# Optimization experiments

Hardware: AMD Instinct MI355X
Metric: run time of the kernel (lower is better)

The kernel has to match this reference:

```python
import jax, jax.numpy as jnp
import numpy as np

B, C, P, NP = 16, 768, 2048, 64
FFE = 4


def _ln(x, g, b, eps=1e-5):
    m = jnp.mean(x, axis=-1, keepdims=True)
    v = jnp.mean(jnp.square(x - m), axis=-1, keepdims=True)
    return (x - m) * jax.lax.rsqrt(v + eps) * g + b


def _gelu(x):
    return jax.nn.gelu(x, approximate=False)  # torch nn.GELU default (erf)


def _any_attn(q, k, v, nqg, nqb, nkg, nkb, nvg, nvb, wq, wk, wv, wp, bq, bk, bv, bp):
    # AnyAttention: LN each stream, project, ReLU-gated logits scaled by d^-0.5, softmax, proj
    scale = q.shape[-1] ** -0.5
    qn = _ln(q, nqg, nqb) @ wq + bq
    kn = _ln(k, nkg, nkb) @ wk + bk
    vn = _ln(v, nvg, nvb) @ wv + bv
    attn = jnp.einsum('bqc,bkc->bqk', qn, kn)
    attn = jax.nn.relu(attn) * scale  # returned attn is relu*scale (pre-softmax)
    out = jnp.einsum('bqk,bkc->bqc', jax.nn.softmax(attn, axis=-1), vn)
    return attn, out @ wp + bp


def _forward(x, parts,
             enc_nq_g, enc_nq_b, enc_nk_g, enc_nk_b, enc_nv_g, enc_nv_b,
             enc_wq, enc_wk, enc_wv, enc_wp, enc_bq, enc_bk, enc_bv, enc_bp,
             dec_nq_g, dec_nq_b, dec_nk_g, dec_nk_b, dec_nv_g, dec_nv_b,
             dec_wq, dec_wk, dec_wv, dec_wp, dec_bq, dec_bk, dec_bv, dec_bp,
             ffn_ng, ffn_nb, ffn_w1, ffn_b1, ffn_w2, ffn_b2,
             sr_w1, sr_b1, sr_w2, sr_b2):
    x = jnp.swapaxes(x, 1, 2)  # b c p -> b p c
    # SimpleReasoning: SE-style gate over part tokens (AdaptiveMaxPool1d(1) = max over channel dim)
    g = jnp.max(parts, axis=-1)                                  # [b, np]
    g = _gelu(g @ sr_w1 + sr_b1)
    gate = jax.nn.sigmoid(g @ sr_w2 + sr_b2)[..., None]          # [b, np, 1]
    parts = gate * parts + parts                                 # parts1 + parts (residual)
    # enc_attn: parts attend over image tokens
    attn0, attn_out = _any_attn(parts, x, x,
                                enc_nq_g, enc_nq_b, enc_nk_g, enc_nk_b, enc_nv_g, enc_nv_b,
                                enc_wq, enc_wk, enc_wv, enc_wp, enc_bq, enc_bk, enc_bv, enc_bp)
    attn_0 = jnp.max(attn0, axis=-1)                             # maxpool over k -> [b, np]
    parts_in = parts + attn_out
    # FFN on image tokens with residual
    h = _ln(x, ffn_ng, ffn_nb)
    feats1 = x + (_gelu(h @ ffn_w1 + ffn_b1) @ ffn_w2 + ffn_b2)
    # dec_attn: image tokens attend over part tokens
    _, feats = _any_attn(feats1, parts_in, parts_in,
                         dec_nq_g, dec_nq_b, dec_nk_g, dec_nk_b, dec_nv_g, dec_nv_b,
                         dec_wq, dec_wk, dec_wv, dec_wp, dec_bq, dec_bk, dec_bv, dec_bp)
    feats = x + feats
    return jnp.swapaxes(feats, 1, 2), attn_0                     # [b, c, p], [b, np]


def setup_inputs() -> dict:
    key = jax.random.key(0)
    ki = iter(jax.random.split(key, 48))
    def rn(shape, s=1.0):
        return jax.random.normal(next(ki), shape, jnp.float32) * s
    d = {}
    d['x'] = rn((B, C, P))
    d['parts'] = rn((B, NP, C))
    for pre in ('enc', 'dec'):
        for nm in ('nq', 'nk', 'nv'):
            d[f'{pre}_{nm}_g'] = jnp.ones((C,), jnp.float32)
            d[f'{pre}_{nm}_b'] = jnp.zeros((C,), jnp.float32)
        for nm in ('wq', 'wk', 'wv', 'wp'):
            d[f'{pre}_{nm}'] = rn((C, C), 0.02)
        for nm in ('bq', 'bk', 'bv', 'bp'):
            d[f'{pre}_{nm}'] = jnp.zeros((C,), jnp.float32)
    d['ffn_ng'] = jnp.ones((C,), jnp.float32)
    d['ffn_nb'] = jnp.zeros((C,), jnp.float32)
    d['ffn_w1'] = rn((C, FFE * C), 0.02)
    d['ffn_b1'] = jnp.zeros((FFE * C,), jnp.float32)
    d['ffn_w2'] = rn((FFE * C, C), 0.02)
    d['ffn_b2'] = jnp.zeros((C,), jnp.float32)
    d['sr_w1'] = rn((NP, NP), 0.1)
    d['sr_b1'] = jnp.zeros((NP,), jnp.float32)
    d['sr_w2'] = rn((NP, NP), 0.1)
    d['sr_b2'] = jnp.zeros((NP,), jnp.float32)
    return d


def reference(x, parts,
              enc_nq_g, enc_nq_b, enc_nk_g, enc_nk_b, enc_nv_g, enc_nv_b,
              enc_wq, enc_wk, enc_wv, enc_wp, enc_bq, enc_bk, enc_bv, enc_bp,
              dec_nq_g, dec_nq_b, dec_nk_g, dec_nk_b, dec_nv_g, dec_nv_b,
              dec_wq, dec_wk, dec_wv, dec_wp, dec_bq, dec_bk, dec_bv, dec_bp,
              ffn_ng, ffn_nb, ffn_w1, ffn_b1, ffn_w2, ffn_b2,
              sr_w1, sr_b1, sr_w2, sr_b2):
    return _forward(x, parts,
                    enc_nq_g, enc_nq_b, enc_nk_g, enc_nk_b, enc_nv_g, enc_nv_b,
                    enc_wq, enc_wk, enc_wv, enc_wp, enc_bq, enc_bk, enc_bv, enc_bp,
                    dec_nq_g, dec_nq_b, dec_nk_g, dec_nk_b, dec_nv_g, dec_nv_b,
                    dec_wq, dec_wk, dec_wv, dec_wp, dec_bq, dec_bk, dec_bv, dec_bp,
                    ffn_ng, ffn_nb, ffn_w1, ffn_b1, ffn_w2, ffn_b2,
                    sr_w1, sr_b1, sr_w2, sr_b2)
```

## Files before the change

kernel.cpp:

```cpp
#include <hip/hip_runtime.h>

typedef unsigned short u16;
typedef unsigned int u32;
typedef __bf16 bf16x8 __attribute__((ext_vector_type(8)));
typedef float f32x4 __attribute__((ext_vector_type(4)));
typedef unsigned int u32x4 __attribute__((ext_vector_type(4)));

#define BB 16
#define CC 768
#define PP 2048
#define FF 3072

__device__ __forceinline__ float b2f(u16 u) {
  unsigned int x = ((unsigned int)u) << 16;
  return __builtin_bit_cast(float, x);
}
__device__ __forceinline__ u16 f2b(float f) {
  unsigned int x = __builtin_bit_cast(unsigned int, f);
  x += 0x7fffu + ((x >> 16) & 1u);
  return (u16)(x >> 16);
}
__device__ __forceinline__ float erf_fast(float x) {
  float ax = fabsf(x);
  float t = 1.0f / fmaf(0.3275911f, ax, 1.0f);
  float p = t * fmaf(t, fmaf(t, fmaf(t, fmaf(t, 1.061405429f, -1.453152027f),
                                     1.421413741f), -0.284496736f), 0.254829592f);
  float r = 1.0f - p * __expf(-ax * ax);
  return copysignf(r, x);
}
__device__ __forceinline__ float gelu_f(float x) {
  return 0.5f * x * (1.0f + erf_fast(x * 0.7071067811865475f));
}

typedef __attribute__((address_space(1))) const unsigned int g_u32;
typedef __attribute__((address_space(3))) unsigned int l_u32;
__device__ __forceinline__ void gl_lds16(const u16* g, u16* l) {
  __builtin_amdgcn_global_load_lds((g_u32*)g, (l_u32*)l, 16, 0, 0);
}

struct Wtr10 {
  const float* W[10]; const float* g[10]; u16* O[10];
  int Kd[10]; int Nd[10]; int tr[10]; int cum[11];
};
__global__ void wtr10_k(Wtr10 a) {
  __shared__ float t[64][65];
  int tbid = blockIdx.x;
  int z = 0;
  while (tbid >= a.cum[z + 1]) ++z;
  int r = tbid - a.cum[z];
  const float* W = a.W[z];
  const float* g = a.g[z];
  u16* Wt = a.O[z];
  int K = a.Kd[z], N = a.Nd[z];
  int nbx = N >> 6;
  int n0 = (r % nbx) * 64, k0 = (r / nbx) * 64;
  int tx = threadIdx.x & 63, ty = threadIdx.x >> 6;
  if (!a.tr[z]) {
    for (int i = 0; i < 16; ++i) {
      int k = k0 + ty + i * 4;
      float sc = g ? g[k] : 1.0f;
      Wt[(long)k * N + n0 + tx] = f2b(W[(long)k * N + n0 + tx] * sc);
    }
    return;
  }
  for (int i = 0; i < 16; ++i) {
    int k = k0 + ty + i * 4;
    float sc = g ? g[k] : 1.0f;
    t[ty + i * 4][tx] = W[(long)k * N + n0 + tx] * sc;
  }
  __syncthreads();
  for (int i = 0; i < 16; ++i) {
    int n = n0 + ty + i * 4;
    Wt[(long)n * K + k0 + tx] = f2b(t[tx][ty + i * 4]);
  }
}

struct Bf7 {
  const float* b[7]; const float* nb[7]; const float* W[7]; float* o[7];
  int Kd[7]; int Nd[7];
};
__global__ void bfuse7_k(Bf7 a) {
  __shared__ float red[4][64];
  int tbid = blockIdx.x;
  int z, bx;
  if (tbid < 72) { z = tbid / 12; bx = tbid % 12; }
  else { z = 6; bx = tbid - 72; }
  const float* b = a.b[z];
  const float* nb = a.nb[z];
  const float* W = a.W[z];
  float* outb = a.o[z];
  int K = a.Kd[z], N = a.Nd[z];
  int n = bx * 64 + (threadIdx.x & 63);
  int slice = threadIdx.x >> 6;
  float acc = 0.f;
#pragma unroll 4
  for (int k = slice; k < K; k += 4) acc += nb[k] * W[(long)k * N + n];
  red[slice][threadIdx.x & 63] = acc;
  __syncthreads();
  if (slice == 0)
    outb[n] = b[n] + red[0][threadIdx.x & 63] + red[1][threadIdx.x & 63] +
              red[2][threadIdx.x & 63] + red[3][threadIdx.x & 63];
}

struct Bf2 { const float* b[2]; const float* nb[2]; const float* W[2]; float* o[2]; };
__global__ void bfuse2_k(Bf2 a) {
  __shared__ float red[4][64];
  int z = blockIdx.x / 12, bx = blockIdx.x % 12;
  const float* b = a.b[z];
  const float* nb = a.nb[z];
  const float* W = a.W[z];
  int n = bx * 64 + (threadIdx.x & 63);
  int slice = threadIdx.x >> 6;
  float acc = 0.f;
#pragma unroll 4
  for (int k = slice; k < CC; k += 4) acc += nb[k] * W[(long)k * CC + n];
  red[slice][threadIdx.x & 63] = acc;
  __syncthreads();
  if (slice == 0)
    a.o[z][n] = (b ? b[n] : 0.f) + red[0][threadIdx.x & 63] +
                red[1][threadIdx.x & 63] + red[2][threadIdx.x & 63] +
                red[3][threadIdx.x & 63];
}

struct Dw4 { const u16* A[4]; const float* v[4]; float* o[4]; };
__global__ void dotw4_k(Dw4 a) {
  int z = blockIdx.x / 192;
  int row = (blockIdx.x % 192) * 4 + (threadIdx.x >> 6);
  int lane = threadIdx.x & 63;
  const u16* ip = a.A[z] + (long)row * CC;
  const float* vec = a.v[z];
  float s = 0.f;
  for (int i = 0; i < 12; ++i) s += b2f(ip[lane + i * 64]) * vec[lane + i * 64];
  for (int o = 32; o; o >>= 1) s += __shfl_xor(s, o);
  if (lane == 0) a.o[z][row] = s;
}

__global__ void scal2_k(const float* a0, const float* b0, float* o0,
                        const float* a1, const float* b1, float* o1) {
  int w = threadIdx.x >> 6, lane = threadIdx.x & 63;
  const float* A = w ? a1 : a0;
  const float* Bv = w ? b1 : b0;
  float s = 0.f;
  for (int i = lane; i < CC; i += 64) s += A[i] * Bv[i];
  for (int o = 32; o; o >>= 1) s += __shfl_xor(s, o);
  if (lane == 0) *(w ? o1 : o0) = s;
}

__global__ void dotc_k(const u16* __restrict__ A, const float* __restrict__ vec,
                       const float* __restrict__ cptr, float* __restrict__ outp) {
  int row = blockIdx.x * 4 + (threadIdx.x >> 6);
  int lane = threadIdx.x & 63;
  const u16* ip = A + (long)row * CC;
  float s = 0.f;
  for (int i = 0; i < 12; ++i) s += b2f(ip[lane + i * 64]) * vec[lane + i * 64];
  for (int o = 32; o; o >>= 1) s += __shfl_xor(s, o);
  if (lane == 0) outp[row] = s + cptr[0];
}

__global__ void xprep_k(const float* __restrict__ x, float* __restrict__ mean,
                        float* __restrict__ rstd, u16* __restrict__ xh) {
  __shared__ float t[64][65];
  __shared__ float red[8][64];
  __shared__ float mn_s[64], rs_s[64];
  int p0 = blockIdx.x * 64, b = blockIdx.y;
  int tx = threadIdx.x & 63, ty = threadIdx.x >> 6;
  const float* xb = x + (long)b * CC * PP;
  float s = 0.f, sq = 0.f;
  for (int c = ty; c < CC; c += 4) {
    float f = xb[(long)c * PP + p0 + tx];
    s += f; sq += f * f;
  }
  red[ty][tx] = s;
  red[4 + ty][tx] = sq;
  __syncthreads();
  if (ty == 0) {
    float S = red[0][tx] + red[1][tx] + red[2][tx] + red[3][tx];
    float Q = red[4][tx] + red[5][tx] + red[6][tx] + red[7][tx];
    float m = S * (1.0f / 768.0f);
    float var = Q * (1.0f / 768.0f) - m * m;
    float rs = rsqrtf(var + 1e-5f);
    mn_s[tx] = m; rs_s[tx] = rs;
    int gi = (b << 11) + p0 + tx;
    mean[gi] = m; rstd[gi] = rs;
  }
  __syncthreads();
  u16* ob = xh + (long)b * PP * CC;
  for (int cb = 0; cb < 12; ++cb) {
    int c0 = cb * 64;
    for (int i = 0; i < 16; ++i)
      t[ty + i * 4][tx] = xb[(long)(c0 + ty + i * 4) * PP + p0 + tx];
    __syncthreads();
    for (int i = 0; i < 16; ++i) {
      int pl = ty + i * 4;
      ob[(long)(p0 + pl) * CC + c0 + tx] = f2b((t[tx][pl] - mn_s[pl]) * rs_s[pl]);
    }
    __syncthreads();
  }
}

__global__ void parts_gate_k(const float* __restrict__ parts,
                             const float* __restrict__ w1, const float* __restrict__ b1,
                             const float* __restrict__ w2, const float* __restrict__ b2,
                             float* __restrict__ gate_out) {
  int b = blockIdx.x, t = threadIdx.x;
  __shared__ float g[64], g1[64];
  int r = t >> 2, l4 = t & 3;
  const float* pr = parts + ((long)b * 64 + r) * CC;
  float m = -1e30f;
  for (int c = l4; c < CC; c += 4) m = fmaxf(m, pr[c]);
  m = fmaxf(m, __shfl_xor(m, 1));
  m = fmaxf(m, __shfl_xor(m, 2));
  if (l4 == 0) g[r] = m;
  __syncthreads();
  if (t < 64) {
    float a = b1[t];
    for (int k = 0; k < 64; ++k) a += g[k] * w1[k * 64 + t];
    g1[t] = gelu_f(a);
  }
  __syncthreads();
  if (t < 64) {
    float a = b2[t];
    for (int k = 0; k < 64; ++k) a += g1[k] * w2[k * 64 + t];
    gate_out[b * 64 + t] = 1.0f / (1.0f + expf(-a));
  }
}

__global__ void gate_ln_k(const float* __restrict__ parts, const float* __restrict__ gate,
                          float* __restrict__ parts1, u16* __restrict__ ph) {
  int row = blockIdx.x * 4 + (threadIdx.x >> 6);
  int lane = threadIdx.x & 63;
  float g = 1.0f + gate[row];
  const float* ip = parts + (long)row * CC;
  float* op1 = parts1 + (long)row * CC;
  float v[12];
  float s = 0.f, sq = 0.f;
  for (int i = 0; i < 12; ++i) {
    float f = ip[lane + i * 64] * g;
    v[i] = f; op1[lane + i * 64] = f;
    s += f; sq += f * f;
  }
  for (int o = 32; o; o >>= 1) { s += __shfl_xor(s, o); sq += __shfl_xor(sq, o); }
  float mean = s * (1.0f / 768.0f);
  float var = sq * (1.0f / 768.0f) - mean * mean;
  float rstd = rsqrtf(var + 1e-5f);
  u16* op = ph + (long)row * CC;
  for (int i = 0; i < 12; ++i) op[lane + i * 64] = f2b((v[i] - mean) * rstd);
}

template <typename T>
__global__ void ln_rows_k(const T* __restrict__ in, u16* __restrict__ outp, int rows) {
  int row = blockIdx.x * 4 + (threadIdx.x >> 6);
  if (row >= rows) return;
  int lane = threadIdx.x & 63;
  const T* ip = in + (long)row * CC;
  float v[12];
  float s = 0.f, sq = 0.f;
  for (int i = 0; i < 12; ++i) {
    float f;
    if constexpr (sizeof(T) == 2) f = b2f(((const u16*)ip)[lane + i * 64]);
    else f = ((const float*)ip)[lane + i * 64];
    v[i] = f; s += f; sq += f * f;
  }
  for (int o = 32; o; o >>= 1) { s += __shfl_xor(s, o); sq += __shfl_xor(sq, o); }
  float mean = s * (1.0f / 768.0f);
  float var = sq * (1.0f / 768.0f) - mean * mean;
  float rstd = rsqrtf(var + 1e-5f);
  u16* op = outp + (long)row * CC;
  for (int i = 0; i < 12; ++i) op[lane + i * 64] = f2b((v[i] - mean) * rstd);
}

__global__ void softmax_enc_k(const float* __restrict__ attn, u16* __restrict__ sm,
                              float* __restrict__ attn0) {
  int row = blockIdx.x * 4 + (threadIdx.x >> 6);
  int lane = threadIdx.x & 63;
  const float* ap = attn + (long)row * PP;
  float v[32];
  float m = -1e30f;
  for (int i = 0; i < 32; ++i) { v[i] = ap[lane + i * 64]; m = fmaxf(m, v[i]); }
  for (int o = 32; o; o >>= 1) m = fmaxf(m, __shfl_xor(m, o));
  float s = 0.f;
  for (int i = 0; i < 32; ++i) { float e = expf(v[i] - m); v[i] = e; s += e; }
  for (int o = 32; o; o >>= 1) s += __shfl_xor(s, o);
  float inv = 1.0f / s;
  u16* sp = sm + (long)row * PP;
  for (int i = 0; i < 32; ++i) sp[lane + i * 64] = f2b(v[i] * inv);
  if (lane == 0) attn0[row] = m;
}

__global__ void pvred_k(const float* __restrict__ part, u16* __restrict__ outp) {
  long i = (long)blockIdx.x * 256 + threadIdx.x;
  const f32x4* p = (const f32x4*)part;
  f32x4 a = p[i];
  a += p[i + 196608];
  a += p[i + 2 * 196608];
  a += p[i + 3 * 196608];
  u32 lo = (u32)f2b(a.x) | ((u32)f2b(a.y) << 16);
  u32 hi = (u32)f2b(a.z) | ((u32)f2b(a.w) << 16);
  ((u32*)outp)[i * 2] = lo;
  ((u32*)outp)[i * 2 + 1] = hi;
}

template <int EPI>
__global__ __launch_bounds__(256) void gemmf_k(
    const u16* __restrict__ A, const u16* __restrict__ Bm, void* __restrict__ Cm,
    const float* __restrict__ bias, int M, int N, int K, int lda,
    const float* __restrict__ res32) {
  __shared__ __align__(16) u16 As[128 * 32];
  __shared__ __align__(16) u16 Bs[128 * 32];
  const int nbx = N >> 7;
  const int nwg = gridDim.x;
  int tile = blockIdx.x;
  if ((nwg & 7) == 0) {
    tile = (tile & 7) * (nwg >> 3) + (tile >> 3);
  }
  const int bm0 = (tile / nbx) << 7;
  const int bn0 = (tile % nbx) << 7;
  const int tid = threadIdx.x;
  const int lane = tid & 63;
  const int wave = tid >> 6;
  const int laneq = lane & 15, lanek = lane >> 4;
  const int wm = (wave >> 1) << 6, wn = (wave & 1) << 6;
  const int srow = wave * 32 + (lane >> 2);
  const int scol = (lane & 3) << 3;
  const u16* Ag0 = A + (long)(bm0 + srow) * lda + scol;
  const u16* Ag1 = A + (long)(bm0 + srow + 16) * lda + scol;
  const u16* Bg0 = Bm + (long)(bn0 + srow) * K + scol;
  const u16* Bg1 = Bm + (long)(bn0 + srow + 16) * K + scol;
  u16* lA0 = As + wave * 1024;
  u16* lA1 = As + wave * 1024 + 512;
  u16* lB0 = Bs + wave * 1024;
  u16* lB1 = Bs + wave * 1024 + 512;
  f32x4 acc[4][4] = {};
  for (int k0 = 0; k0 < K; k0 += 32) {
    gl_lds16(Ag0 + k0, lA0);
    gl_lds16(Ag1 + k0, lA1);
    gl_lds16(Bg0 + k0, lB0);
    gl_lds16(Bg1 + k0, lB1);
    __syncthreads();
    bf16x8 af[4], bfr[4];
#pragma unroll
    for (int i = 0; i < 4; ++i)
      af[i] = *(const bf16x8*)(As + (wm + i * 16 + laneq) * 32 + (lanek << 3));
#pragma unroll
    for (int i = 0; i < 4; ++i)
      bfr[i] = *(const bf16x8*)(Bs + (wn + i * 16 + laneq) * 32 + (lanek << 3));
#pragma unroll
    for (int mi = 0; mi < 4; ++mi)
#pragma unroll
      for (int ni = 0; ni < 4; ++ni)
        acc[mi][ni] =
            __builtin_amdgcn_mfma_f32_16x16x32_bf16(af[mi], bfr[ni], acc[mi][ni], 0, 0, 0);
    __syncthreads();
  }
#pragma unroll
  for (int mi = 0; mi < 4; ++mi) {
#pragma unroll
    for (int r = 0; r < 4; ++r) {
      const int row = bm0 + wm + mi * 16 + (lanek << 2) + r;
#pragma unroll
      for (int ni = 0; ni < 4; ++ni) {
        const int col = bn0 + wn + ni * 16 + laneq;
        float v = acc[mi][ni][r] + (bias ? bias[col] : 0.f);
        long off = (long)row * N + col;
        if constexpr (EPI == 0) {
          ((u16*)Cm)[off] = f2b(v);
        } else if constexpr (EPI == 1) {
          ((u16*)Cm)[off] = f2b(gelu_f(v));
        } else {
          ((float*)Cm)[off] = v + res32[off];
        }
      }
    }
  }
}

struct G4 { const u16* A[4]; const u16* B[4]; u16* C[4]; };
__global__ __launch_bounds__(256) void gemmf4_k(G4 a) {
  __shared__ __align__(16) u16 As[128 * 32];
  __shared__ __align__(16) u16 Bs[128 * 32];
  const int z = blockIdx.x / 36;
  const int r = blockIdx.x % 36;
  const u16* A = a.A[z];
  const u16* Bm = a.B[z];
  u16* Cm = a.C[z];
  const int bm0 = (r / 6) << 7;
  const int bn0 = (r % 6) << 7;
  const int tid = threadIdx.x;
  const int lane = tid & 63;
  const int wave = tid >> 6;
  const int laneq = lane & 15, lanek = lane >> 4;
  const int wm = (wave >> 1) << 6, wn = (wave & 1) << 6;
  const int srow = wave * 32 + (lane >> 2);
  const int scol = (lane & 3) << 3;
  const u16* Ag0 = A + (long)(bm0 + srow) * CC + scol;
  const u16* Ag1 = A + (long)(bm0 + srow + 16) * CC + scol;
  const u16* Bg0 = Bm + (long)(bn0 + srow) * CC + scol;
  const u16* Bg1 = Bm + (long)(bn0 + srow + 16) * CC + scol;
  u16* lA0 = As + wave * 1024;
  u16* lA1 = As + wave * 1024 + 512;
  u16* lB0 = Bs + wave * 1024;
  u16* lB1 = Bs + wave * 1024 + 512;
  f32x4 acc[4][4] = {};
  for (int k0 = 0; k0 < CC; k0 += 32) {
    gl_lds16(Ag0 + k0, lA0);
    gl_lds16(Ag1 + k0, lA1);
    gl_lds16(Bg0 + k0, lB0);
    gl_lds16(Bg1 + k0, lB1);
    __syncthreads();
    bf16x8 af[4], bfr[4];
#pragma unroll
    for (int i = 0; i < 4; ++i)
      af[i] = *(const bf16x8*)(As + (wm + i * 16 + laneq) * 32 + (lanek << 3));
#pragma unroll
    for (int i = 0; i < 4; ++i)
      bfr[i] = *(const bf16x8*)(Bs + (wn + i * 16 + laneq) * 32 + (lanek << 3));
#pragma unroll
    for (int mi = 0; mi < 4; ++mi)
#pragma unroll
      for (int ni = 0; ni < 4; ++ni)
        acc[mi][ni] =
            __builtin_amdgcn_mfma_f32_16x16x32_bf16(af[mi], bfr[ni], acc[mi][ni], 0, 0, 0);
    __syncthreads();
  }
#pragma unroll
  for (int mi = 0; mi < 4; ++mi)
#pragma unroll
    for (int r2 = 0; r2 < 4; ++r2) {
      const int row = bm0 + wm + mi * 16 + (lanek << 2) + r2;
#pragma unroll
      for (int ni = 0; ni < 4; ++ni) {
        const int col = bn0 + wn + ni * 16 + laneq;
        Cm[(long)row * CC + col] = f2b(acc[mi][ni][r2]);
      }
    }
}

#define G256_BAR() __builtin_amdgcn_s_barrier()
#define G256_WLGKM0()                                    \
  do {                                                   \
    asm volatile("s_waitcnt lgkmcnt(0)" ::: "memory");   \
    __builtin_amdgcn_sched_barrier(0);                   \
  } while (0)
#define G256_RD_A(HALF)                                                        \
  _Pragma("unroll") for (int m2 = 0; m2 < 4; ++m2) {                           \
    af[m2 * 2 + 0] = *(const bf16x8*)(Ab + ar + (HALF)*4096 + m2 * 1024 + g0); \
    af[m2 * 2 + 1] = *(const bf16x8*)(Ab + ar + (HALF)*4096 + m2 * 1024 + g1); \
  }
#define G256_RD_B(HALF, BFR)                                                   \
  _Pragma("unroll") for (int n2 = 0; n2 < 2; ++n2) {                           \
    BFR[n2 * 2 + 0] = *(const bf16x8*)(Bb + br + (HALF)*2048 + n2 * 1024 + g0);\
    BFR[n2 * 2 + 1] = *(const bf16x8*)(Bb + br + (HALF)*2048 + n2 * 1024 + g1);\
  }
#define G256_MFMA_Q(H, NH, BFR)                                                \
  __builtin_amdgcn_s_setprio(1);                                               \
  _Pragma("unroll") for (int m2 = 0; m2 < 4; ++m2)                             \
  _Pragma("unroll") for (int n2 = 0; n2 < 2; ++n2)                             \
  _Pragma("unroll") for (int s = 0; s < 2; ++s)                                \
      acc[(H)*4 + m2][(NH)*2 + n2] = __builtin_amdgcn_mfma_f32_16x16x32_bf16(  \
          af[m2 * 2 + s], BFR[n2 * 2 + s], acc[(H)*4 + m2][(NH)*2 + n2], 0, 0, 0); \
  __builtin_amdgcn_s_setprio(0);

template <int EPI>
__global__ __launch_bounds__(512, 2) void gemm256_k(
    const u16* __restrict__ A, const u16* __restrict__ Bm, void* __restrict__ Cm,
    const float* __restrict__ bias, int M, int N, int K,
    const u16* __restrict__ rxh, const float* __restrict__ rmean,
    const float* __restrict__ rrstd, long rro, int nbm) {
  __shared__ __align__(16) u16 As[2 * 16384];
  __shared__ __align__(16) u16 Bs[2 * 16384];
  const int nbx = N >> 8;
  const int nwg = gridDim.x;
  int tile = blockIdx.x;
  if ((nwg & 7) == 0) {
    tile = (tile & 7) * (nwg >> 3) + (tile >> 3);
  }
  int bm0, bn0;
  if (nbm) {
    bm0 = (tile % nbm) << 8;
    bn0 = (tile / nbm) << 8;
  } else {
    bm0 = (tile / nbx) << 8;
    bn0 = (tile % nbx) << 8;
  }
  const int tid = threadIdx.x;
  const int lane = tid & 63;
  const int wave = tid >> 6;
  const int laneq = lane & 15, lanek = lane >> 4;
  const int wrow = (wave >> 2) << 7;
  const int wcol = (wave & 3) << 6;
  const int srow8 = lane >> 3;
  const int sg = (lane & 7) ^ srow8;
  const u16* gA = A + (long)(bm0 + wave * 8 + srow8) * K + sg * 8;
  const u16* gB = Bm + (long)(bn0 + wave * 8 + srow8) * K + sg * 8;
  const long lineK = (long)64 * K;
  const int ldsLine = wave * 512;
  const int gx = laneq & 7;
  const int g0 = ((lanek) ^ gx) << 3;
  const int g1 = ((lanek + 4) ^ gx) << 3;
  const int ar = (wrow + laneq) * 64;
  const int br = (wcol + laneq) * 64;
  f32x4 acc[8][4] = {};
  bf16x8 af[8], bfr0[4], bfr1[4];
  const int NT = K >> 6;

  {
    u16* dA = (u16*)As;
    u16* dB = (u16*)Bs;
    gl_lds16(gA, dA + ldsLine);
    gl_lds16(gA + lineK, dA + ldsLine + 4096);
    gl_lds16(gA + 2 * lineK, dA + ldsLine + 8192);
    gl_lds16(gA + 3 * lineK, dA + ldsLine + 12288);
    gl_lds16(gB, dB + ldsLine);
    gl_lds16(gB + lineK, dB + ldsLine + 4096);
    gl_lds16(gB + 2 * lineK, dB + ldsLine + 8192);
    gl_lds16(gB + 3 * lineK, dB + ldsLine + 12288);
  }
  for (int T = 0; T < NT; ++T) {
    const u16* Ab = As + (T & 1) * 16384;
    const u16* Bb = Bs + (T & 1) * 16384;
    u16* An = (u16*)As + ((T & 1) ^ 1) * 16384;
    u16* Bn = (u16*)Bs + ((T & 1) ^ 1) * 16384;
    const long ko = (long)(T + 1) * 64;
    const bool more = (T + 1 < NT);
    if (more) {
      gl_lds16(gA + ko, An + ldsLine);
      gl_lds16(gA + ko + lineK, An + ldsLine + 4096);
      gl_lds16(gB + ko, Bn + ldsLine);
      gl_lds16(gB + ko + lineK, Bn + ldsLine + 4096);
      asm volatile("s_waitcnt vmcnt(4)" ::: "memory");
    } else {
      asm volatile("s_waitcnt vmcnt(0)" ::: "memory");
    }
    G256_BAR();
    G256_RD_A(0);
    G256_RD_B(0, bfr0);
    G256_WLGKM0();
    G256_MFMA_Q(0, 0, bfr0);
    G256_BAR();
    if (more) {
      gl_lds16(gA + ko + 2 * lineK, An + ldsLine + 8192);
      gl_lds16(gA + ko + 3 * lineK, An + ldsLine + 12288);
      gl_lds16(gB + ko + 2 * lineK, Bn + ldsLine + 8192);
      gl_lds16(gB + ko + 3 * lineK, Bn + ldsLine + 12288);
    }
    G256_RD_B(1, bfr1);
    G256_BAR();
    G256_WLGKM0();
    G256_MFMA_Q(0, 1, bfr1);
    G256_BAR();
    G256_RD_A(1);
    G256_BAR();
    G256_WLGKM0();
    G256_MFMA_Q(1, 1, bfr1);
    G256_BAR();
    G256_MFMA_Q(1, 0, bfr0);
  }

#pragma unroll
  for (int mi = 0; mi < 8; ++mi) {
#pragma unroll
    for (int r = 0; r < 4; ++r) {
      const int row = bm0 + wrow + mi * 16 + (lanek << 2) + r;
      float mn = 0.f, istd = 0.f;
      if constexpr (EPI == 3) {
        long gr = rro + row;
        mn = rmean[gr];
        istd = 1.0f / rrstd[gr];
      }
#pragma unroll
      for (int ni = 0; ni < 4; ++ni) {
        const int col = bn0 + wcol + ni * 16 + laneq;
        float v = acc[mi][ni][r] + bias[col];
        long off = (long)row * N + col;
        if constexpr (EPI == 0) {
          ((u16*)Cm)[off] = f2b(v);
        } else if constexpr (EPI == 1) {
          ((u16*)Cm)[off] = f2b(gelu_f(v));
        } else {
          v += b2f(rxh[(rro + row) * 768 + col]) * istd + mn;
          ((u16*)Cm)[off] = f2b(v);
        }
      }
    }
  }
}

template <int EPI, bool BNT, int TM, int TN>
__global__ __launch_bounds__(256) void gemm_k(
    const u16* __restrict__ A, const u16* __restrict__ Bm, void* __restrict__ Cm,
    const float* __restrict__ bias, int M, int N, int kLen, int lda, int ldB,
    long sA, long sB, long sC, float scale, const float* __restrict__ res32,
    const float* __restrict__ radd) {
  __shared__ __align__(16) u16 As[TM][40];
  __shared__ __align__(16) u16 Bs[TN][40];
  const int bn0 = blockIdx.x * TN;
  const int bm0 = (EPI == 4) ? 0 : blockIdx.y * TM;
  const int kOff = (EPI == 4) ? blockIdx.y * kLen : 0;
  const int bz = blockIdx.z;
  const u16* Ab = A + (long)bz * sA;
  const u16* Bb = Bm + (long)bz * sB;
  const long coff = (EPI == 4) ? ((long)blockIdx.y * gridDim.z + bz) * sC
                               : (long)bz * sC;
  const int tid = threadIdx.x;
  const int lane = tid & 63;
  const int wave = tid >> 6;
  const int wm = (TM == 64) ? 0 : ((TN == 64) ? wave * 32 : ((wave >> 1) << 6));
  const int wn = (TN == 64) ? 0 : ((TM == 64) ? wave * 32 : ((wave & 1) << 6));
  constexpr int MI = (TN == 64) ? 2 : 4;
  constexpr int NI = (TM == 64) ? 2 : 4;
  const int laneq = lane & 15, lanek = lane >> 4;
  f32x4 acc[MI][NI] = {};
  for (int k0 = 0; k0 < kLen; k0 += 32) {
    __syncthreads();
#pragma unroll
    for (int j = 0; j < TM / 64; ++j) {
      int v = tid + j * 256;
      int m = v >> 2, kcl = (v & 3) << 3;
      u32x4 val = {0, 0, 0, 0};
      if (bm0 + m < M)
        val = *(const u32x4*)(Ab + (long)(bm0 + m) * lda + kOff + k0 + kcl);
      *(u32x4*)(&As[m][kcl]) = val;
    }
    if constexpr (BNT) {
#pragma unroll
      for (int j = 0; j < TN / 64; ++j) {
        int v = tid + j * 256;
        int n = v >> 2, kcl = (v & 3) << 3;
        u32x4 val = {0, 0, 0, 0};
        if (bn0 + n < N)
          val = *(const u32x4*)(Bb + (long)(bn0 + n) * ldB + kOff + k0 + kcl);
        *(u32x4*)(&Bs[n][kcl]) = val;
      }
    } else {
      constexpr int CCH = TN / 8;
#pragma unroll
      for (int j = 0; j < TN / 64; ++j) {
        int v = tid + j * 256;
        int kk = v / CCH, nc = (v % CCH) << 3;
        u32x4 val = {0, 0, 0, 0};
        if (bn0 + nc < N)
          val = *(const u32x4*)(Bb + (long)(kOff + k0 + kk) * ldB + bn0 + nc);
        union { u32x4 v4; u16 u[8]; } uu;
        uu.v4 = val;
#pragma unroll
        for (int e = 0; e < 8; ++e) Bs[nc + e][kk] = uu.u[e];
      }
    }
    __syncthreads();
    bf16x8 af[MI], bfr[NI];
#pragma unroll
    for (int i = 0; i < MI; ++i)
      af[i] = *(const bf16x8*)(&As[wm + i * 16 + laneq][lanek << 3]);
#pragma unroll
    for (int i = 0; i < NI; ++i)
      bfr[i] = *(const bf16x8*)(&Bs[wn + i * 16 + laneq][lanek << 3]);
#pragma unroll
    for (int mi = 0; mi < MI; ++mi)
#pragma unroll
      for (int ni = 0; ni < NI; ++ni)
        acc[mi][ni] =
            __builtin_amdgcn_mfma_f32_16x16x32_bf16(af[mi], bfr[ni], acc[mi][ni], 0, 0, 0);
  }
  if constexpr (EPI == 5) {
    __syncthreads();
    float* smem = (float*)(wave < 2 ? (void*)As : (void*)Bs) + (wave & 1) * 1024;
    const int pbase = bm0 + wm + (lane & 3) * 16;
    const long obase = (long)bz * CC * PP;
#pragma unroll
    for (int ni = 0; ni < 4; ++ni) {
#pragma unroll
      for (int mi = 0; mi < 4; ++mi)
#pragma unroll
        for (int r = 0; r < 4; ++r) {
          const int col = bn0 + wn + ni * 16 + laneq;
          smem[(mi * 16 + (lanek << 2) + r) * 16 + laneq] = acc[mi][ni][r] + bias[col];
        }
      const int c = bn0 + wn + ni * 16 + (lane >> 2);
      const float* xs = res32 + obase + (long)c * PP + pbase;
      float* os = (float*)Cm + obase + (long)c * PP + pbase;
      const float* sr = smem + (lane & 3) * 256 + (lane >> 2);
#pragma unroll
      for (int q4 = 0; q4 < 4; ++q4) {
        f32x4 xv = *(const f32x4*)(xs + q4 * 4);
        f32x4 ov;
        ov.x = sr[(q4 * 4 + 0) * 16] + xv.x;
        ov.y = sr[(q4 * 4 + 1) * 16] + xv.y;
        ov.z = sr[(q4 * 4 + 2) * 16] + xv.z;
        ov.w = sr[(q4 * 4 + 3) * 16] + xv.w;
        *(f32x4*)(os + q4 * 4) = ov;
      }
    }
  } else if constexpr (EPI == 6) {
#pragma unroll
    for (int mi = 0; mi < MI; ++mi) {
#pragma unroll
      for (int r = 0; r < 4; ++r) {
        float e[NI];
        float mx = -1e30f;
#pragma unroll
        for (int ni = 0; ni < NI; ++ni) {
          const int col = bn0 + wn + ni * 16 + laneq;
          float v = acc[mi][ni][r] + (radd ? radd[(long)bz * N + col] : 0.f);
          v = fmaxf(v, 0.0f) * scale;
          e[ni] = v;
          mx = fmaxf(mx, v);
        }
        mx = fmaxf(mx, __shfl_xor(mx, 1));
        mx = fmaxf(mx, __shfl_xor(mx, 2));
        mx = fmaxf(mx, __shfl_xor(mx, 4));
        mx = fmaxf(mx, __shfl_xor(mx, 8));
        float s = 0.f;
#pragma unroll
        for (int ni = 0; ni < NI; ++ni) { e[ni] = __expf(e[ni] - mx); s += e[ni]; }
        s += __shfl_xor(s, 1);
        s += __shfl_xor(s, 2);
        s += __shfl_xor(s, 4);
        s += __shfl_xor(s, 8);
        float inv = 1.0f / s;
        const int row = bm0 + wm + mi * 16 + (lanek << 2) + r;
#pragma unroll
        for (int ni = 0; ni < NI; ++ni) {
          const int col = bn0 + wn + ni * 16 + laneq;
          ((u16*)Cm)[coff + (long)row * N + col] = f2b(e[ni] * inv);
        }
      }
    }
  } else {
#pragma unroll
    for (int mi = 0; mi < MI; ++mi) {
#pragma unroll
      for (int ni = 0; ni < NI; ++ni) {
        int col = bn0 + wn + ni * 16 + laneq;
        if (col >= N) continue;
#pragma unroll
        for (int r = 0; r < 4; ++r) {
          int row = bm0 + wm + mi * 16 + (lanek << 2) + r;
          if (row >= M) continue;
          float v = acc[mi][ni][r];
          long off = coff + (long)row * N + col;
          if constexpr (EPI == 2) {
            v += radd ? radd[(long)bz * M + row] : 0.f;
            ((float*)Cm)[off] = fmaxf(v, 0.0f) * scale;
          } else {
            ((float*)Cm)[off] = v;
          }
        }
      }
    }
  }
}

extern "C" void kernel_launch(void* const* d_in, const int* in_sizes, int n_in,
                              void* d_out, int out_size, void* d_ws, size_t ws_size,
                              hipStream_t stream) {
  (void)in_sizes; (void)n_in; (void)out_size;
  const float* x        = (const float*)d_in[0];
  const float* parts    = (const float*)d_in[1];
  const float* enc_nq_g = (const float*)d_in[2];
  const float* enc_nq_b = (const float*)d_in[3];
  const float* enc_nk_g = (const float*)d_in[4];
  const float* enc_nk_b = (const float*)d_in[5];
  const float* enc_nv_g = (const float*)d_in[6];
  const float* enc_nv_b = (const float*)d_in[7];
  const float* enc_wq   = (const float*)d_in[8];
  const float* enc_wk   = (const float*)d_in[9];
  const float* enc_wv   = (const float*)d_in[10];
  const float* enc_wp   = (const float*)d_in[11];
  const float* enc_bq   = (const float*)d_in[12];
  const float* enc_bk   = (const float*)d_in[13];
  const float* enc_bv   = (const float*)d_in[14];
  const float* enc_bp   = (const float*)d_in[15];
  const float* dec_nq_g = (const float*)d_in[16];
  const float* dec_nq_b = (const float*)d_in[17];
  const float* dec_nk_g = (const float*)d_in[18];
  const float* dec_nk_b = (const float*)d_in[19];
  const float* dec_nv_g = (const float*)d_in[20];
  const float* dec_nv_b = (const float*)d_in[21];
  const float* dec_wq   = (const float*)d_in[22];
  const float* dec_wk   = (const float*)d_in[23];
  const float* dec_wv   = (const float*)d_in[24];
  const float* dec_wp   = (const float*)d_in[25];
  const float* dec_bq   = (const float*)d_in[26];
  const float* dec_bk   = (const float*)d_in[27];
  const float* dec_bv   = (const float*)d_in[28];
  const float* dec_bp   = (const float*)d_in[29];
  const float* ffn_ng   = (const float*)d_in[30];
  const float* ffn_nb   = (const float*)d_in[31];
  const float* ffn_w1   = (const float*)d_in[32];
  const float* ffn_b1   = (const float*)d_in[33];
  const float* ffn_w2   = (const float*)d_in[34];
  const float* ffn_b2   = (const float*)d_in[35];
  const float* sr_w1    = (const float*)d_in[36];
  const float* sr_b1    = (const float*)d_in[37];
  const float* sr_w2    = (const float*)d_in[38];
  const float* sr_b2    = (const float*)d_in[39];
  float* outp = (float*)d_out;

  char* base = (char*)d_ws;
  size_t used = 0;
  auto alloc = [&](size_t bytes) -> void* {
    void* p = base + used;
    used += (bytes + 255) & ~(size_t)255;
    return p;
  };
  const long MC = (long)CC * CC;
  u16* WpeT = (u16*)alloc(MC * 2);
  u16* WpdT = (u16*)alloc(MC * 2);
  u16* W1T  = (u16*)alloc((long)CC * FF * 2);
  u16* W2T  = (u16*)alloc((long)CC * FF * 2);
  u16* WkR  = (u16*)alloc(MC * 2);
  u16* WqR  = (u16*)alloc(MC * 2);
  u16* WvS  = (u16*)alloc(MC * 2);
  u16* WqdR = (u16*)alloc(MC * 2);
  u16* WkdR = (u16*)alloc(MC * 2);
  u16* WvdR = (u16*)alloc(MC * 2);
  u16* m2w  = (u16*)alloc(MC * 2);
  u16* Bqk  = (u16*)alloc(MC * 2);
  u16* Bgv  = (u16*)alloc(MC * 2 * 2);
  float* bqe  = (float*)alloc(CC * 4);
  float* bke  = (float*)alloc(CC * 4);
  float* bve  = (float*)alloc(CC * 4);
  float* bqd  = (float*)alloc(CC * 4);
  float* bkd  = (float*)alloc(CC * 4);
  float* bvd  = (float*)alloc(CC * 4);
  float* b1f  = (float*)alloc(FF * 4);
  float* bias2   = (float*)alloc(CC * 4);
  float* bias_gv = (float*)alloc(2 * CC * 4);
  float* bq2     = (float*)alloc(CC * 4);
  float* wqb     = (float*)alloc(CC * 4);
  float* wkb     = (float*)alloc(CC * 4);
  float* cq      = (float*)alloc(256);
  float* ck      = (float*)alloc(256);
  float* meanx = (float*)alloc((long)BB * PP * 4);
  float* rstdx = (float*)alloc((long)BB * PP * 4);
  const long BPC = (long)BB * PP * CC;
  u16* bufA = (u16*)alloc(BPC * 2);
  u16* bufB = (u16*)alloc(BPC * 2);
  const long PC = (long)BB * 64 * CC;
  float* parts1   = (float*)alloc(PC * 4);
  float* gateb    = (float*)alloc((long)BB * 64 * 4);
  u16*   p1hat    = (u16*)alloc(PC * 2);
  u16*   qtil     = (u16*)alloc(PC * 2);
  float* qdotv    = (float*)alloc((long)BB * 64 * 4);
  float* attn_e   = (float*)alloc((long)BB * 64 * PP * 4);
  u16*   sm_e     = (u16*)alloc((long)BB * 64 * PP * 2);
  u16*   pv_e     = (u16*)alloc(PC * 2);
  float* pvpart   = (float*)alloc((long)4 * PC * 4);
  float* parts_in = (float*)alloc(PC * 4);
  u16*   pin_hat  = (u16*)alloc(PC * 2);
  u16*   GVW      = (u16*)alloc(PC * 2 * 2);
  float* kdotv    = (float*)alloc((long)BB * 64 * 4);
  u16*   sm_d     = (u16*)alloc((long)BB * PP * 64 * 2);
  int chunk_rows = 16384;
  while (chunk_rows > 4096 &&
         used + (size_t)chunk_rows * FF * 2 > ws_size)
    chunk_rows >>= 1;
  u16* ff1 = (u16*)alloc((long)chunk_rows * FF * 2);
  if (used > ws_size) return;

  const float scale = 0.03608439182435161f;
  dim3 blk(256);
  dim3 blk2(512);

  {
    Wtr10 wa;
    const float* Ws[10] = {enc_wp, dec_wp, ffn_w1, ffn_w2, enc_wk,
                           enc_wq, enc_wv, dec_wq, dec_wk, dec_wv};
    const float* gs[10] = {nullptr, nullptr, ffn_ng, nullptr, enc_nk_g,
                           enc_nq_g, enc_nv_g, dec_nq_g, dec_nk_g, dec_nv_g};
    u16* Os[10] = {WpeT, WpdT, W1T, W2T, WkR, WqR, WvS, WqdR, WkdR, WvdR};
    int Ks[10] = {CC, CC, CC, FF, CC, CC, CC, CC, CC, CC};
    int Ns[10] = {CC, CC, FF, CC, CC, CC, CC, CC, CC, CC};
    int tr[10] = {1, 1, 1, 1, 0, 0, 0, 0, 0, 0};
    int cum = 0;
    for (int i = 0; i < 10; ++i) {
      wa.W[i] = Ws[i]; wa.g[i] = gs[i]; wa.O[i] = Os[i];
      wa.Kd[i] = Ks[i]; wa.Nd[i] = Ns[i]; wa.tr[i] = tr[i];
      wa.cum[i] = cum;
      cum += (Ns[i] / 64) * (Ks[i] / 64);
    }
    wa.cum[10] = cum;
    wtr10_k<<<cum, blk, 0, stream>>>(wa);
    Bf7 ba;
    const float* bs[7] = {enc_bq, enc_bk, enc_bv, dec_bq, dec_bk, dec_bv, ffn_b1};
    const float* nbs[7] = {enc_nq_b, enc_nk_b, enc_nv_b, dec_nq_b, dec_nk_b,
                           dec_nv_b, ffn_nb};
    const float* ws[7] = {enc_wq, enc_wk, enc_wv, dec_wq, dec_wk, dec_wv, ffn_w1};
    float* os[7] = {bqe, bke, bve, bqd, bkd, bvd, b1f};
    for (int i = 0; i < 7; ++i) {
      ba.b[i] = bs[i]; ba.nb[i] = nbs[i]; ba.W[i] = ws[i]; ba.o[i] = os[i];
      ba.Kd[i] = CC; ba.Nd[i] = (i == 6) ? FF : CC;
    }
    bfuse7_k<<<120, blk, 0, stream>>>(ba);
    Bf2 b2a;
    b2a.b[0] = enc_bp;  b2a.nb[0] = bve; b2a.W[0] = enc_wp; b2a.o[0] = bias2;
    b2a.b[1] = nullptr; b2a.nb[1] = bvd; b2a.W[1] = dec_wp; b2a.o[1] = bias_gv + CC;
    bfuse2_k<<<24, blk, 0, stream>>>(b2a);
    Dw4 da;
    da.A[0] = WkR;  da.v[0] = bqe; da.o[0] = bq2;
    da.A[1] = WqR;  da.v[1] = bke; da.o[1] = wqb;
    da.A[2] = WqdR; da.v[2] = bkd; da.o[2] = bias_gv;
    da.A[3] = WkdR; da.v[3] = bqd; da.o[3] = wkb;
    dotw4_k<<<768, blk, 0, stream>>>(da);
    scal2_k<<<1, 128, 0, stream>>>(bqe, bke, cq, bkd, bqd, ck);
    G4 ga;
    ga.A[0] = WpeT; ga.B[0] = WvS;  ga.C[0] = m2w;
    ga.A[1] = WkR;  ga.B[1] = WqR;  ga.C[1] = Bqk;
    ga.A[2] = WqdR; ga.B[2] = WkdR; ga.C[2] = Bgv;
    ga.A[3] = WpdT; ga.B[3] = WvdR; ga.C[3] = Bgv + MC;
    gemmf4_k<<<144, blk, 0, stream>>>(ga);
  }

  xprep_k<<<dim3(32, 16), blk, 0, stream>>>(x, meanx, rstdx, bufA);

  parts_gate_k<<<16, blk, 0, stream>>>(parts, sr_w1, sr_b1, sr_w2, sr_b2, gateb);
  gate_ln_k<<<256, blk, 0, stream>>>(parts, gateb, parts1, p1hat);

  gemmf_k<0><<<48, blk, 0, stream>>>(p1hat, Bqk, qtil, bq2, 1024, CC, CC, CC,
      nullptr);
  dotc_k<<<256, blk, 0, stream>>>(p1hat, wqb, cq, qdotv);

  gemm_k<2, true, 64, 128><<<dim3(16, 1, 16), blk, 0, stream>>>(
      qtil, bufA, attn_e, nullptr, 64, PP, CC, CC, CC,
      (long)64 * CC, (long)PP * CC, (long)64 * PP, scale, nullptr, qdotv);
  softmax_enc_k<<<256, blk, 0, stream>>>(attn_e, sm_e, outp + (long)BB * CC * PP);
  gemm_k<4, false, 64, 128><<<dim3(6, 4, 16), blk, 0, stream>>>(
      sm_e, bufA, pvpart, nullptr, 64, CC, PP / 4, PP, CC,
      (long)64 * PP, (long)PP * CC, (long)64 * CC, 0.f, nullptr, nullptr);
  pvred_k<<<768, blk, 0, stream>>>(pvpart, pv_e);
  gemmf_k<4><<<48, blk, 0, stream>>>(pv_e, m2w, parts_in, bias2, 1024, CC, CC, CC,
      parts1);

  ln_rows_k<float><<<256, blk, 0, stream>>>(parts_in, pin_hat, 1024);
  gemmf_k<0><<<96, blk, 0, stream>>>(pin_hat, Bgv, GVW, bias_gv, 1024, 2 * CC, CC,
      CC, nullptr);
  dotc_k<<<256, blk, 0, stream>>>(pin_hat, wkb, ck, kdotv);

  for (long r0 = 0; r0 < 32768; r0 += chunk_rows) {
    gemmf_k<1><<<(chunk_rows / 128) * 24, blk, 0, stream>>>(
        bufA + r0 * CC, W1T, ff1, b1f, chunk_rows, FF, CC, CC, nullptr);
    gemm256_k<3><<<(chunk_rows / 256) * 3, blk2, 0, stream>>>(
        ff1, W2T, bufB + r0 * CC, ffn_b2, chunk_rows, CC, FF,
        bufA, meanx, rstdx, r0, 0);
  }
  ln_rows_k<u16><<<8192, blk, 0, stream>>>(bufB, bufB, 32768);

  gemm_k<6, true, 128, 64><<<dim3(1, 16, 16), blk, 0, stream>>>(
      bufB, GVW, sm_d, nullptr, PP, 64, CC, CC, 2 * CC,
      (long)PP * CC, (long)64 * 2 * CC, (long)PP * 64, scale, nullptr, kdotv);

  gemm_k<5, false, 128, 128><<<dim3(6, 16, 16), blk, 0, stream>>>(
      sm_d, GVW + CC, outp, dec_bp, PP, CC, 64, 64, 2 * CC,
      (long)PP * 64, (long)64 * 2 * CC, 0, 0.f, x, nullptr);
}
```

Baseline: 1.077 ms.

## Fuse decoder attention into one kernel and route FFN1 through 256-tile GEMM

The decoder attention's logits+softmax GEMM and its PV+residual GEMM are merged into a single kernel. The softmax probabilities stay in LDS instead of going through a global sm_d buffer, and V is staged once per batch. The FFN first-layer GEMM with GELU now uses the larger 256x256 pipelined gemm256 kernel instead of the 128-tile gemmf kernel. The scalar-dot kernel is also folded into an extra block of bfuse2 to save a launch. The fused decoder kernel launches only 256 blocks with heavy LDS use, which may limit occupancy.

Result: faster. 1.019 ms (-5.4%).

```diff
diff --git a/kernel.cpp b/kernel.cpp
--- a/kernel.cpp
+++ b/kernel.cpp
@@ -102,8 +102,24 @@
               red[2][threadIdx.x & 63] + red[3][threadIdx.x & 63];
 }
 
-struct Bf2 { const float* b[2]; const float* nb[2]; const float* W[2]; float* o[2]; };
+struct Bf2 {
+  const float* b[2]; const float* nb[2]; const float* W[2]; float* o[2];
+  const float* sa0; const float* sb0; float* so0;
+  const float* sa1; const float* sb1; float* so1;
+};
 __global__ void bfuse2_k(Bf2 a) {
+  if (blockIdx.x == 24) {
+    if (threadIdx.x < 128) {
+      int w = threadIdx.x >> 6, lane = threadIdx.x & 63;
+      const float* A = w ? a.sa1 : a.sa0;
+      const float* Bv = w ? a.sb1 : a.sb0;
+      float s = 0.f;
+      for (int i = lane; i < CC; i += 64) s += A[i] * Bv[i];
+      for (int o = 32; o; o >>= 1) s += __shfl_xor(s, o);
+      if (lane == 0) *(w ? a.so1 : a.so0) = s;
+    }
+    return;
+  }
   __shared__ float red[4][64];
   int z = blockIdx.x / 12, bx = blockIdx.x % 12;
   const float* b = a.b[z];
@@ -133,17 +149,6 @@
   for (int i = 0; i < 12; ++i) s += b2f(ip[lane + i * 64]) * vec[lane + i * 64];
   for (int o = 32; o; o >>= 1) s += __shfl_xor(s, o);
   if (lane == 0) a.o[z][row] = s;
-}
-
-__global__ void scal2_k(const float* a0, const float* b0, float* o0,
-                        const float* a1, const float* b1, float* o1) {
-  int w = threadIdx.x >> 6, lane = threadIdx.x & 63;
-  const float* A = w ? a1 : a0;
-  const float* Bv = w ? b1 : b0;
-  float s = 0.f;
-  for (int i = lane; i < CC; i += 64) s += A[i] * Bv[i];
-  for (int o = 32; o; o >>= 1) s += __shfl_xor(s, o);
-  if (lane == 0) *(w ? o1 : o0) = s;
 }
 
 __global__ void dotc_k(const u16* __restrict__ A, const float* __restrict__ vec,
@@ -364,8 +369,6 @@
         long off = (long)row * N + col;
         if constexpr (EPI == 0) {
           ((u16*)Cm)[off] = f2b(v);
-        } else if constexpr (EPI == 1) {
-          ((u16*)Cm)[off] = f2b(gelu_f(v));
         } else {
           ((float*)Cm)[off] = v + res32[off];
         }
@@ -465,7 +468,7 @@
     const u16* __restrict__ A, const u16* __restrict__ Bm, void* __restrict__ Cm,
     const float* __restrict__ bias, int M, int N, int K,
     const u16* __restrict__ rxh, const float* __restrict__ rmean,
-    const float* __restrict__ rrstd, long rro, int nbm) {
+    const float* __restrict__ rrstd, long rro) {
   __shared__ __align__(16) u16 As[2 * 16384];
   __shared__ __align__(16) u16 Bs[2 * 16384];
   const int nbx = N >> 8;
@@ -474,14 +477,8 @@
   if ((nwg & 7) == 0) {
     tile = (tile & 7) * (nwg >> 3) + (tile >> 3);
   }
-  int bm0, bn0;
-  if (nbm) {
-    bm0 = (tile % nbm) << 8;
-    bn0 = (tile / nbm) << 8;
-  } else {
-    bm0 = (tile / nbx) << 8;
-    bn0 = (tile % nbx) << 8;
-  }
+  const int bm0 = (tile / nbx) << 8;
+  const int bn0 = (tile % nbx) << 8;
   const int tid = threadIdx.x;
   const int lane = tid & 63;
   const int wave = tid >> 6;
@@ -661,23 +658,156 @@
         acc[mi][ni] =
             __builtin_amdgcn_mfma_f32_16x16x32_bf16(af[mi], bfr[ni], acc[mi][ni], 0, 0, 0);
   }
-  if constexpr (EPI == 5) {
+#pragma unroll
+  for (int mi = 0; mi < MI; ++mi) {
+#pragma unroll
+    for (int ni = 0; ni < NI; ++ni) {
+      int col = bn0 + wn + ni * 16 + laneq;
+      if (col >= N) continue;
+#pragma unroll
+      for (int r = 0; r < 4; ++r) {
+        int row = bm0 + wm + mi * 16 + (lanek << 2) + r;
+        if (row >= M) continue;
+        float v = acc[mi][ni][r];
+        long off = coff + (long)row * N + col;
+        if constexpr (EPI == 2) {
+          v += radd ? radd[(long)bz * M + row] : 0.f;
+          ((float*)Cm)[off] = fmaxf(v, 0.0f) * scale;
+        } else {
+          ((float*)Cm)[off] = v;
+        }
+      }
+    }
+  }
+}
+
+__global__ __launch_bounds__(256) void decattn_k(
+    const u16* __restrict__ fh, const u16* __restrict__ GVW,
+    const float* __restrict__ kdotv, const float* __restrict__ x,
+    const float* __restrict__ bias, float* __restrict__ outp, float scale) {
+  __shared__ __align__(16) u16 As[128][40];
+  __shared__ __align__(16) u16 Bs[64][40];
+  __shared__ __align__(16) u16 Vs[768][68];
+  __shared__ __align__(16) u16 Ps[128][72];
+  __shared__ float Ts[4][1024];
+  const int bm0 = blockIdx.x * 128;
+  const int bz = blockIdx.y;
+  const int tid = threadIdx.x, lane = tid & 63, wave = tid >> 6;
+  const int laneq = lane & 15, lanek = lane >> 4;
+  {
+    const u16* vw = GVW + ((long)bz * 64) * 1536 + 768;
+    for (int it = 0; it < 24; ++it) {
+      int l8 = tid + it * 256;
+      int j = l8 / 96;
+      int c8 = (l8 % 96) * 8;
+      union { bf16x8 v; u16 u[8]; } uu;
+      uu.v = *(const bf16x8*)(vw + (long)j * 1536 + c8);
+#pragma unroll
+      for (int e = 0; e < 8; ++e) Vs[c8 + e][j] = uu.u[e];
+    }
+  }
+  const u16* Ab = fh + (long)bz * PP * CC;
+  const u16* Bb = GVW + (long)bz * 64 * 1536;
+  const int wm = wave * 32;
+  f32x4 acc[2][4] = {};
+  for (int k0 = 0; k0 < CC; k0 += 32) {
     __syncthreads();
-    float* smem = (float*)(wave < 2 ? (void*)As : (void*)Bs) + (wave & 1) * 1024;
-    const int pbase = bm0 + wm + (lane & 3) * 16;
-    const long obase = (long)bz * CC * PP;
+#pragma unroll
+    for (int j = 0; j < 2; ++j) {
+      int v = tid + j * 256;
+      int m = v >> 2, kcl = (v & 3) << 3;
+      *(u32x4*)(&As[m][kcl]) =
+          *(const u32x4*)(Ab + (long)(bm0 + m) * CC + k0 + kcl);
+    }
+    {
+      int n = tid >> 2, kcl = (tid & 3) << 3;
+      *(u32x4*)(&Bs[n][kcl]) = *(const u32x4*)(Bb + (long)n * 1536 + k0 + kcl);
+    }
+    __syncthreads();
+    bf16x8 af[2], bfr[4];
+#pragma unroll
+    for (int i = 0; i < 2; ++i)
+      af[i] = *(const bf16x8*)(&As[wm + i * 16 + laneq][lanek << 3]);
+#pragma unroll
+    for (int i = 0; i < 4; ++i)
+      bfr[i] = *(const bf16x8*)(&Bs[i * 16 + laneq][lanek << 3]);
+#pragma unroll
+    for (int mi = 0; mi < 2; ++mi)
+#pragma unroll
+      for (int ni = 0; ni < 4; ++ni)
+        acc[mi][ni] =
+            __builtin_amdgcn_mfma_f32_16x16x32_bf16(af[mi], bfr[ni], acc[mi][ni], 0, 0, 0);
+  }
+#pragma unroll
+  for (int mi = 0; mi < 2; ++mi) {
+#pragma unroll
+    for (int r = 0; r < 4; ++r) {
+      float e[4];
+      float mx = -1e30f;
+#pragma unroll
+      for (int ni = 0; ni < 4; ++ni) {
+        const int col = ni * 16 + laneq;
+        float v = acc[mi][ni][r] + kdotv[(long)bz * 64 + col];
+        v = fmaxf(v, 0.0f) * scale;
+        e[ni] = v;
+        mx = fmaxf(mx, v);
+      }
+      mx = fmaxf(mx, __shfl_xor(mx, 1));
+      mx = fmaxf(mx, __shfl_xor(mx, 2));
+      mx = fmaxf(mx, __shfl_xor(mx, 4));
+      mx = fmaxf(mx, __shfl_xor(mx, 8));
+      float s = 0.f;
+#pragma unroll
+      for (int ni = 0; ni < 4; ++ni) { e[ni] = __expf(e[ni] - mx); s += e[ni]; }
+      s += __shfl_xor(s, 1);
+      s += __shfl_xor(s, 2);
+      s += __shfl_xor(s, 4);
+      s += __shfl_xor(s, 8);
+      float inv = 1.0f / s;
+      const int prow = wm + mi * 16 + (lanek << 2) + r;
+#pragma unroll
+      for (int ni = 0; ni < 4; ++ni)
+        Ps[prow][ni * 16 + laneq] = f2b(e[ni] * inv);
+    }
+  }
+  __syncthreads();
+  const int wr = (wave & 1) << 6;
+  const int wc = (wave >> 1) << 6;
+  const long obase = (long)bz * CC * PP;
+  const int pbase = bm0 + wr + (lane & 3) * 16;
+  for (int nc = 0; nc < 6; ++nc) {
+    f32x4 a2[4][4] = {};
+#pragma unroll
+    for (int ks = 0; ks < 2; ++ks) {
+      bf16x8 af[4], bfr[4];
+#pragma unroll
+      for (int i = 0; i < 4; ++i)
+        af[i] = *(const bf16x8*)(&Ps[wr + i * 16 + laneq][ks * 32 + (lanek << 3)]);
+#pragma unroll
+      for (int i = 0; i < 4; ++i)
+        bfr[i] = *(const bf16x8*)(&Vs[nc * 128 + wc + i * 16 + laneq]
+                                     [ks * 32 + (lanek << 3)]);
+#pragma unroll
+      for (int mi = 0; mi < 4; ++mi)
+#pragma unroll
+        for (int ni = 0; ni < 4; ++ni)
+          a2[mi][ni] =
+              __builtin_amdgcn_mfma_f32_16x16x32_bf16(af[mi], bfr[ni], a2[mi][ni], 0, 0, 0);
+    }
+    float* smem = Ts[wave];
 #pragma unroll
     for (int ni = 0; ni < 4; ++ni) {
 #pragma unroll
       for (int mi = 0; mi < 4; ++mi)
 #pragma unroll
         for (int r = 0; r < 4; ++r) {
-          const int col = bn0 + wn + ni * 16 + laneq;
-          smem[(mi * 16 + (lanek << 2) + r) * 16 + laneq] = acc[mi][ni][r] + bias[col];
+          const int col = nc * 128 + wc + ni * 16 + laneq;
+          smem[(mi * 16 + (lanek << 2) + r) * 16 + laneq] =
+              a2[mi][ni][r] + bias[col];
         }
-      const int c = bn0 + wn + ni * 16 + (lane >> 2);
-      const float* xs = res32 + obase + (long)c * PP + pbase;
-      float* os = (float*)Cm + obase + (long)c * PP + pbase;
+      const int c = nc * 128 + wc + ni * 16 + (lane >> 2);
+      const float* xs = x + obase + (long)c * PP + pbase;
+      float* os = outp + obase + (long)c * PP + pbase;
       const float* sr = smem + (lane & 3) * 256 + (lane >> 2);
 #pragma unroll
       for (int q4 = 0; q4 < 4; ++q4) {
@@ -688,63 +818,6 @@
         ov.z = sr[(q4 * 4 + 2) * 16] + xv.z;
         ov.w = sr[(q4 * 4 + 3) * 16] + xv.w;
         *(f32x4*)(os + q4 * 4) = ov;
-      }
-    }
-  } else if constexpr (EPI == 6) {
-#pragma unroll
-    for (int mi = 0; mi < MI; ++mi) {
-#pragma unroll
-      for (int r = 0; r < 4; ++r) {
-        float e[NI];
-        float mx = -1e30f;
-#pragma unroll
-        for (int ni = 0; ni < NI; ++ni) {
-          const int col = bn0 + wn + ni * 16 + laneq;
-          float v = acc[mi][ni][r] + (radd ? radd[(long)bz * N + col] : 0.f);
-          v = fmaxf(v, 0.0f) * scale;
-          e[ni] = v;
-          mx = fmaxf(mx, v);
-        }
-        mx = fmaxf(mx, __shfl_xor(mx, 1));
-        mx = fmaxf(mx, __shfl_xor(mx, 2));
-        mx = fmaxf(mx, __shfl_xor(mx, 4));
-        mx = fmaxf(mx, __shfl_xor(mx, 8));
-        float s = 0.f;
-#pragma unroll
-        for (int ni = 0; ni < NI; ++ni) { e[ni] = __expf(e[ni] - mx); s += e[ni]; }
-        s += __shfl_xor(s, 1);
-        s += __shfl_xor(s, 2);
-        s += __shfl_xor(s, 4);
-        s += __shfl_xor(s, 8);
-        float inv = 1.0f / s;
-        const int row = bm0 + wm + mi * 16 + (lanek << 2) + r;
-#pragma unroll
-        for (int ni = 0; ni < NI; ++ni) {
-          const int col = bn0 + wn + ni * 16 + laneq;
-          ((u16*)Cm)[coff + (long)row * N + col] = f2b(e[ni] * inv);
-        }
-      }
-    }
-  } else {
-#pragma unroll
-    for (int mi = 0; mi < MI; ++mi) {
-#pragma unroll
-      for (int ni = 0; ni < NI; ++ni) {
-        int col = bn0 + wn + ni * 16 + laneq;
-        if (col >= N) continue;
-#pragma unroll
-        for (int r = 0; r < 4; ++r) {
-          int row = bm0 + wm + mi * 16 + (lanek << 2) + r;
-          if (row >= M) continue;
-          float v = acc[mi][ni][r];
-          long off = coff + (long)row * N + col;
-          if constexpr (EPI == 2) {
-            v += radd ? radd[(long)bz * M + row] : 0.f;
-            ((float*)Cm)[off] = fmaxf(v, 0.0f) * scale;
-          } else {
-            ((float*)Cm)[off] = v;
-          }
-        }
       }
     }
   }
@@ -850,7 +923,6 @@
   u16*   pin_hat  = (u16*)alloc(PC * 2);
   u16*   GVW      = (u16*)alloc(PC * 2 * 2);
   float* kdotv    = (float*)alloc((long)BB * 64 * 4);
-  u16*   sm_d     = (u16*)alloc((long)BB * PP * 64 * 2);
   int chunk_rows = 16384;
   while (chunk_rows > 4096 &&
          used + (size_t)chunk_rows * FF * 2 > ws_size)
@@ -895,14 +967,15 @@
     Bf2 b2a;
     b2a.b[0] = enc_bp;  b2a.nb[0] = bve; b2a.W[0] = enc_wp; b2a.o[0] = bias2;
     b2a.b[1] = nullptr; b2a.nb[1] = bvd; b2a.W[1] = dec_wp; b2a.o[1] = bias_gv + CC;
-    bfuse2_k<<<24, blk, 0, stream>>>(b2a);
+    b2a.sa0 = bqe; b2a.sb0 = bke; b2a.so0 = cq;
+    b2a.sa1 = bkd; b2a.sb1 = bqd; b2a.so1 = ck;
+    bfuse2_k<<<25, blk, 0, stream>>>(b2a);
     Dw4 da;
     da.A[0] = WkR;  da.v[0] = bqe; da.o[0] = bq2;
     da.A[1] = WqR;  da.v[1] = bke; da.o[1] = wqb;
     da.A[2] = WqdR; da.v[2] = bkd; da.o[2] = bias_gv;
     da.A[3] = WkdR; da.v[3] = bqd; da.o[3] = wkb;
     dotw4_k<<<768, blk, 0, stream>>>(da);
-    scal2_k<<<1, 128, 0, stream>>>(bqe, bke, cq, bkd, bqd, ck);
     G4 ga;
     ga.A[0] = WpeT; ga.B[0] = WvS;  ga.C[0] = m2w;
     ga.A[1] = WkR;  ga.B[1] = WqR;  ga.C[1] = Bqk;
@@ -937,19 +1010,15 @@
   dotc_k<<<256, blk, 0, stream>>>(pin_hat, wkb, ck, kdotv);
 
   for (long r0 = 0; r0 < 32768; r0 += chunk_rows) {
-    gemmf_k<1><<<(chunk_rows / 128) * 24, blk, 0, stream>>>(
-        bufA + r0 * CC, W1T, ff1, b1f, chunk_rows, FF, CC, CC, nullptr);
+    gemm256_k<1><<<(chunk_rows / 256) * 12, blk2, 0, stream>>>(
+        bufA + r0 * CC, W1T, ff1, b1f, chunk_rows, FF, CC,
+        nullptr, nullptr, nullptr, 0);
     gemm256_k<3><<<(chunk_rows / 256) * 3, blk2, 0, stream>>>(
         ff1, W2T, bufB + r0 * CC, ffn_b2, chunk_rows, CC, FF,
-        bufA, meanx, rstdx, r0, 0);
+        bufA, meanx, rstdx, r0);
   }
   ln_rows_k<u16><<<8192, blk, 0, stream>>>(bufB, bufB, 32768);
 
-  gemm_k<6, true, 128, 64><<<dim3(1, 16, 16), blk, 0, stream>>>(
-      bufB, GVW, sm_d, nullptr, PP, 64, CC, CC, 2 * CC,
-      (long)PP * CC, (long)64 * 2 * CC, (long)PP * 64, scale, nullptr, kdotv);
-
-  gemm_k<5, false, 128, 128><<<dim3(6, 16, 16), blk, 0, stream>>>(
-      sm_d, GVW + CC, outp, dec_bp, PP, CC, 64, 64, 2 * CC,
-      (long)PP * 64, (long)64 * 2 * CC, 0, 0.f, x, nullptr);
-}
+  decattn_k<<<dim3(16, 16), blk, 0, stream>>>(
+      bufB, GVW, kdotv, x, dec_bp, outp, scale);
+}
```
